# Performance work log

Measured on AMD Instinct MI355X. Metric: run time of the kernel, lower is better.

Reference implementation:

```python
import jax, jax.numpy as jnp
import numpy as np
from jax import lax

B, N, C = 16, 16384, 256          # batch, points, seed feature dim
P, NS = 256, 16                   # num_proposal, ball-query nsample
RADIUS = 0.3
NUM_CLASS, NUM_HEADING_BIN, NUM_SIZE = 18, 12, 18
OUT_FEAT = 2 + 3 + NUM_HEADING_BIN * 2 + NUM_SIZE * 4 + NUM_CLASS   # 119
PN2_NC = 128
MID_FEAT = (PN2_NC + OUT_FEAT) // 2                                 # 123
EPS = 1e-5

PARAM_NAMES = [f"mlp_{s}{i}" for i in range(3) for s in ("w", "b", "g", "be")] + [
    "c1_w", "c1_b", "bn1_g", "bn1_b", "c2_w", "c2_b", "bn2_g", "bn2_b", "c3_w", "c3_b"]


def setup_inputs():
    key = jax.random.key(0)
    ks = iter(jax.random.split(key, 32))
    def w(shape):
        return jax.random.normal(next(ks), shape, jnp.float32) / np.float32(np.sqrt(shape[0]))
    inp = {
        "pos":      jax.random.normal(next(ks), (B, N, 3), jnp.float32),
        "features": jax.random.normal(next(ks), (B, C, N), jnp.float32),
        "seed_pos": jax.random.normal(next(ks), (B, N, 3), jnp.float32),
    }
    dims = [3 + C, PN2_NC, PN2_NC, PN2_NC]
    for i in range(3):
        inp[f"mlp_w{i}"]  = w((dims[i], dims[i + 1]))
        inp[f"mlp_b{i}"]  = jnp.zeros((dims[i + 1],), jnp.float32)
        inp[f"mlp_g{i}"]  = jnp.ones((dims[i + 1],), jnp.float32)
        inp[f"mlp_be{i}"] = jnp.zeros((dims[i + 1],), jnp.float32)
    inp["c1_w"], inp["c1_b"] = w((PN2_NC, PN2_NC)), jnp.zeros((PN2_NC,), jnp.float32)
    inp["bn1_g"], inp["bn1_b"] = jnp.ones((PN2_NC,), jnp.float32), jnp.zeros((PN2_NC,), jnp.float32)
    inp["c2_w"], inp["c2_b"] = w((PN2_NC, MID_FEAT)), jnp.zeros((MID_FEAT,), jnp.float32)
    inp["bn2_g"], inp["bn2_b"] = jnp.ones((MID_FEAT,), jnp.float32), jnp.zeros((MID_FEAT,), jnp.float32)
    inp["c3_w"], inp["c3_b"] = w((MID_FEAT, OUT_FEAT)), jnp.zeros((OUT_FEAT,), jnp.float32)
    return inp


def _fps(p):
    # iterative furthest point sampling on one cloud p:[N,3] -> [P] int32 (starts at index 0)
    def step(carry, _):
        dists, far = carry
        d = jnp.sum((p - p[far]) ** 2, axis=-1)
        dists = jnp.minimum(dists, d)
        return (dists, jnp.argmax(dists).astype(jnp.int32)), far
    init = (jnp.full((p.shape[0],), 1e10, p.dtype), jnp.array(0, jnp.int32))
    _, idx = lax.scan(step, init, None, length=P)
    return idx


def _ball_query(new_pos, pos):
    # first NS points of pos within RADIUS of each center (CUDA ball_query semantics)
    d2 = jnp.sum((new_pos[:, :, None, :] - pos[:, None, :, :]) ** 2, -1)  # [B,P,N]
    n = pos.shape[1]
    ar = jnp.arange(n, dtype=jnp.int32)
    sortkey = jnp.where(d2 <= RADIUS ** 2, ar, ar + n)
    vals, idx = lax.top_k(-sortkey, NS)        # smallest keys = earliest in-radius indices
    valid = (-vals) < n
    return jnp.where(valid, idx, idx[..., :1])  # pad misses with first hit


def _bn(x, g, b, axes):
    m = jnp.mean(x, axes, keepdims=True)
    v = jnp.var(x, axes, keepdims=True)
    return (x - m) * lax.rsqrt(v + EPS) * g + b


def _forward(pos, features, seed_pos, params):
    idx_p = jax.vmap(_fps)(seed_pos)                              # seed_fps sampling [B,P]
    take = jax.vmap(lambda a, i: a[i])
    new_pos = take(pos, idx_p)                                    # [B,P,3]
    idx = _ball_query(new_pos, pos)                               # [B,P,NS]
    gp = take(pos, idx.reshape(B, -1)).reshape(B, P, NS, 3)
    gf = take(features.transpose(0, 2, 1), idx.reshape(B, -1)).reshape(B, P, NS, C)
    x = jnp.concatenate([gp - new_pos[:, :, None, :], gf], -1)    # [B,P,NS,3+C]
    for i in range(3):                                            # shared MLP (1x1 conv2d + BN + ReLU)
        x = jax.nn.relu(_bn(x @ params[f"mlp_w{i}"] + params[f"mlp_b{i}"],
                            params[f"mlp_g{i}"], params[f"mlp_be{i}"], (0, 1, 2)))
    x = jnp.max(x, axis=2)                                        # max over neighbors -> [B,P,128]
    x = jax.nn.relu(_bn(x @ params["c1_w"] + params["c1_b"], params["bn1_g"], params["bn1_b"], (0, 1)))
    x = jax.nn.relu(_bn(x @ params["c2_w"] + params["c2_b"], params["bn2_g"], params["bn2_b"], (0, 1)))
    x = x @ params["c3_w"] + params["c3_b"]                       # [B,P,OUT_FEAT]
    return x.transpose(0, 2, 1)                                   # [B,OUT_FEAT,P] like torch Conv1d


def reference(pos, features, seed_pos, mlp_w0, mlp_b0, mlp_g0, mlp_be0, mlp_w1, mlp_b1, mlp_g1, mlp_be1, mlp_w2, mlp_b2, mlp_g2, mlp_be2, c1_w, c1_b, bn1_g, bn1_b, c2_w, c2_b, bn2_g, bn2_b, c3_w, c3_b):
    ps = [mlp_w0, mlp_b0, mlp_g0, mlp_be0, mlp_w1, mlp_b1, mlp_g1, mlp_be1,
          mlp_w2, mlp_b2, mlp_g2, mlp_be2, c1_w, c1_b, bn1_g, bn1_b,
          c2_w, c2_b, bn2_g, bn2_b, c3_w, c3_b]
    params = dict(zip(PARAM_NAMES, ps))
    return _forward(pos, features, seed_pos, params)
```

## Files before the change

### kernel.cpp

```cpp
#include <hip/hip_runtime.h>

#define N_PTS 16384
#define BATCH 16
#define NPROP 256
#define NSAMP 16
#define CFEAT 256
#define KIN 259
#define KPAD 264
#define MBIG 65536
#define MSMALL 4096
#define NOUT 119
#define NBLK_BIG 512
#define NBLK_SMALL 64

#define FPS_LIST(M) M(0) M(1) M(2) M(3) M(4) M(5) M(6) M(7) \
  M(8) M(9) M(10) M(11) M(12) M(13) M(14) M(15) \
  M(16) M(17) M(18) M(19) M(20) M(21) M(22) M(23) \
  M(24) M(25) M(26) M(27) M(28) M(29) M(30) M(31)

#define FPS_PIN8(a,b,c,d,e,f,g,h) \
  asm volatile("" : "+v"(a), "+v"(b), "+v"(c), "+v"(d), \
                    "+v"(e), "+v"(f), "+v"(g), "+v"(h));

__global__ __attribute__((amdgpu_flat_work_group_size(512,512), amdgpu_waves_per_eu(2,2)))
void fps_kernel(const float* __restrict__ sp, const float* __restrict__ pos,
                int* __restrict__ idx_p, float* __restrict__ npos) {
#pragma clang fp contract(off)
  const int b = blockIdx.x;
  const int t = threadIdx.x;
  const int w = t >> 6;
  const int lane = t & 63;
  const float* base = sp + (size_t)b * N_PTS * 3;

#define FPS_DECL(J) float px##J, py##J, pz##J, dd##J;
  FPS_LIST(FPS_DECL)
#undef FPS_DECL

#define FPS_INIT(J) { const int i = t + J*512; \
    px##J = base[i*3+0]; py##J = base[i*3+1]; pz##J = base[i*3+2]; \
    dd##J = 1e10f; }
  FPS_LIST(FPS_INIT)
#undef FPS_INIT

  FPS_PIN8(px0,px1,px2,px3,px4,px5,px6,px7)
  FPS_PIN8(px8,px9,px10,px11,px12,px13,px14,px15)
  FPS_PIN8(px16,px17,px18,px19,px20,px21,px22,px23)
  FPS_PIN8(px24,px25,px26,px27,px28,px29,px30,px31)
  FPS_PIN8(py0,py1,py2,py3,py4,py5,py6,py7)
  FPS_PIN8(py8,py9,py10,py11,py12,py13,py14,py15)
  FPS_PIN8(py16,py17,py18,py19,py20,py21,py22,py23)
  FPS_PIN8(py24,py25,py26,py27,py28,py29,py30,py31)
  FPS_PIN8(pz0,pz1,pz2,pz3,pz4,pz5,pz6,pz7)
  FPS_PIN8(pz8,pz9,pz10,pz11,pz12,pz13,pz14,pz15)
  FPS_PIN8(pz16,pz17,pz18,pz19,pz20,pz21,pz22,pz23)
  FPS_PIN8(pz24,pz25,pz26,pz27,pz28,pz29,pz30,pz31)

  __shared__ unsigned long long part[2][8];
  __shared__ int sidx[NPROP];
  if (t == 0) { idx_p[b*NPROP] = 0; sidx[0] = 0; }
  float fx = base[0], fy = base[1], fz = base[2];
  for (int it = 1; it < NPROP; ++it) {
    float mv = -1.0f; int mi = 0;
#define FPS_STEP(J) { \
    float dx = px##J - fx, dy = py##J - fy, dz = pz##J - fz; \
    float d = (dx*dx + dy*dy) + dz*dz; \
    float nd = fminf(dd##J, d); \
    dd##J = nd; \
    if (nd > mv) { mv = nd; mi = t + J*512; } }
    FPS_LIST(FPS_STEP)
#undef FPS_STEP
    unsigned long long key =
      ((unsigned long long)__float_as_uint(mv) << 32) |
      (unsigned long long)(unsigned)(0x7FFFFFFF - mi);
#pragma unroll
    for (int o = 32; o > 0; o >>= 1) {
      unsigned long long ok = __shfl_xor(key, o, 64);
      if (ok > key) key = ok;
    }
    const int buf = it & 1;
    if (lane == 0) part[buf][w] = key;
    __syncthreads();
    unsigned long long k2 = part[buf][0];
#pragma unroll
    for (int q = 1; q < 8; ++q) {
      unsigned long long ok = part[buf][q];
      if (ok > k2) k2 = ok;
    }
    const int far = 0x7FFFFFFF - (int)(unsigned)(k2 & 0xFFFFFFFFull);
    if (t == 0) { idx_p[b*NPROP + it] = far; sidx[it] = far; }
    const float* fp = base + (size_t)far*3;
    fx = fp[0]; fy = fp[1]; fz = fp[2];
  }
  __syncthreads();
  if (t < NPROP) {
    const int ii = sidx[t];
    const float* pp = pos + ((size_t)b*N_PTS + ii)*3;
    float* np = npos + (size_t)(b*NPROP + t)*3;
    np[0] = pp[0]; np[1] = pp[1]; np[2] = pp[2];
  }
}

__global__ __launch_bounds__(256)
void ballq_kernel(const float* __restrict__ pos, const float* __restrict__ npos,
                  int* __restrict__ idxg) {
#pragma clang fp contract(off)
  __shared__ int res[4][NSAMP];
  const int tid = threadIdx.x;
  const int w = tid >> 6, lane = tid & 63;
  const int cid = blockIdx.x*4 + w;
  const int b = cid >> 8;
  const float R2 = (float)(0.3*0.3);
  if (lane == 0) res[w][0] = 0;
  const float cx = npos[cid*3+0], cy = npos[cid*3+1], cz = npos[cid*3+2];
  const float* pb = pos + (size_t)b*N_PTS*3;
  int cnt = 0;
  const unsigned long long lmask = (1ull << lane) - 1ull;
#pragma unroll 4
  for (int ch = 0; ch < N_PTS/64; ++ch) {
    int i = ch*64 + lane;
    float dx = pb[i*3+0]-cx, dy = pb[i*3+1]-cy, dz = pb[i*3+2]-cz;
    float d2 = (dx*dx + dy*dy) + dz*dz;
    bool pred = d2 <= R2;
    unsigned long long bal = __ballot(pred);
    if (pred) {
      int slot = cnt + (int)__popcll(bal & lmask);
      if (slot < NSAMP) res[w][slot] = i;
    }
    cnt += (int)__popcll(bal);
  }
  __syncthreads();
  if (lane < NSAMP) {
    int v = res[w][lane];
    if (lane >= cnt) v = res[w][0];
    idxg[cid*NSAMP + lane] = v;
  }
}

__global__ __launch_bounds__(256)
void prep_w(const float* __restrict__ w0, const float* __restrict__ c2w,
            const float* __restrict__ c2b, const float* __restrict__ c3w,
            const float* __restrict__ c3b,
            float* __restrict__ Wp0, float* __restrict__ Wp2, float* __restrict__ B2p,
            float* __restrict__ Wp3, float* __restrict__ B3p) {
  int g = blockIdx.x*256 + threadIdx.x;
  const int S0 = KPAD*128, S1 = S0 + 16384, S2 = S1 + 128, S3 = S2 + 16384, S4 = S3 + 128;
  if (g < S0) {
    int k = g >> 7, n = g & 127;
    Wp0[g] = (k < KIN) ? w0[k*128 + n] : 0.f;
  } else if (g < S1) {
    int g2 = g - S0; int k = g2 >> 7, n = g2 & 127;
    Wp2[g2] = (n < 123) ? c2w[k*123 + n] : 0.f;
  } else if (g < S2) {
    int n = g - S1;
    B2p[n] = (n < 123) ? c2b[n] : 0.f;
  } else if (g < S3) {
    int g2 = g - S2; int k = g2 >> 7, n = g2 & 127;
    Wp3[g2] = (k < 123 && n < NOUT) ? c3w[k*NOUT + n] : 0.f;
  } else if (g < S4) {
    int n = g - S3;
    B3p[n] = (n < NOUT) ? c3b[n] : 0.f;
  }
}

__global__ __launch_bounds__(256)
void gemm_l0(const float* __restrict__ pos, const float* __restrict__ npos,
             const float* __restrict__ feat, const int* __restrict__ idxg,
             const float* __restrict__ Wp, const float* __restrict__ bias,
             float* __restrict__ H, float* __restrict__ Sp, float* __restrict__ Qp) {
  __shared__ float As[8][128];
  __shared__ float Ws[8][128];
  __shared__ float pd[3][128];
  __shared__ int ids[128];
  const int tid = threadIdx.x;
  const int m0 = blockIdx.x * 128;
  const int b = m0 >> 12;
  const float* fb = feat + (size_t)b * CFEAT * N_PTS;
  if (tid < 128) {
    int m = m0 + tid;
    int ii = idxg[m];
    ids[tid] = ii;
    int q = m >> 4;
    const float* pp = pos + ((size_t)b*N_PTS + ii)*3;
    const float* cc = npos + (size_t)q*3;
    pd[0][tid] = pp[0] - cc[0];
    pd[1][tid] = pp[1] - cc[1];
    pd[2][tid] = pp[2] - cc[2];
  }
  __syncthreads();
  const int kr = tid >> 5;
  const int cm = (tid & 31) * 4;
  int ii_r[4];
#pragma unroll
  for (int x = 0; x < 4; ++x) ii_r[x] = ids[cm+x];
  float acc[8][8];
#pragma unroll
  for (int i = 0; i < 8; ++i)
#pragma unroll
    for (int j = 0; j < 8; ++j) acc[i][j] = 0.f;
  const int tm = tid & 15, tn = tid >> 4;
  for (int k0 = 0; k0 < KPAD; k0 += 8) {
    const int k = k0 + kr;
    float4 a0;
    if (k < 3) {
      a0.x = pd[k][cm+0]; a0.y = pd[k][cm+1]; a0.z = pd[k][cm+2]; a0.w = pd[k][cm+3];
    } else if (k < KIN) {
      const float* fr = fb + (size_t)(k-3)*N_PTS;
      a0.x = fr[ii_r[0]]; a0.y = fr[ii_r[1]]; a0.z = fr[ii_r[2]]; a0.w = fr[ii_r[3]];
    } else {
      a0 = make_float4(0.f,0.f,0.f,0.f);
    }
    float4 wv = *(const float4*)(Wp + (size_t)k*128 + cm);
    __syncthreads();
    *(float4*)&As[kr][cm] = a0;
    *(float4*)&Ws[kr][cm] = wv;
    __syncthreads();
#pragma unroll
    for (int kk = 0; kk < 8; ++kk) {
      float a[8], bb[8];
      *(float4*)(a)   = *(const float4*)&As[kk][tm*4];
      *(float4*)(a+4) = *(const float4*)&As[kk][tm*4 + 64];
      *(float4*)(bb)   = *(const float4*)&Ws[kk][tn*8];
      *(float4*)(bb+4) = *(const float4*)&Ws[kk][tn*8+4];
#pragma unroll
      for (int i = 0; i < 8; ++i)
#pragma unroll
        for (int j = 0; j < 8; ++j)
          acc[i][j] = fmaf(a[i], bb[j], acc[i][j]);
    }
  }
#pragma unroll
  for (int j = 0; j < 8; ++j) {
    const int n = tn*8 + j;
    const float bv = bias[n];
    float* cr = H + (size_t)n*MBIG + m0 + tm*4;
    float4 o0, o1;
    o0.x = acc[0][j]+bv; o0.y = acc[1][j]+bv; o0.z = acc[2][j]+bv; o0.w = acc[3][j]+bv;
    o1.x = acc[4][j]+bv; o1.y = acc[5][j]+bv; o1.z = acc[6][j]+bv; o1.w = acc[7][j]+bv;
    *(float4*)(cr)      = o0;
    *(float4*)(cr + 64) = o1;
    float s = o0.x+o0.y+o0.z+o0.w + o1.x+o1.y+o1.z+o1.w;
    float q = o0.x*o0.x+o0.y*o0.y+o0.z*o0.z+o0.w*o0.w
            + o1.x*o1.x+o1.y*o1.y+o1.z*o1.z+o1.w*o1.w;
#pragma unroll
    for (int o = 1; o < 16; o <<= 1) {
      s += __shfl_xor(s, o, 64);
      q += __shfl_xor(q, o, 64);
    }
    if (tm == 0) {
      Sp[(size_t)n*NBLK_BIG + blockIdx.x] = s;
      Qp[(size_t)n*NBLK_BIG + blockIdx.x] = q;
    }
  }
}

template<int TM, int MODE, int DOPART>
__global__ __launch_bounds__(256)
void gemm_k(const float* __restrict__ A, const float* __restrict__ W,
            const float* __restrict__ bias, const float* __restrict__ sc,
            const float* __restrict__ sh, float* __restrict__ C,
            float* __restrict__ Sp, float* __restrict__ Qp,
            int M, int K, int useT) {
  __shared__ float As[8][TM];
  __shared__ float Ws[8][128];
  const int tid = threadIdx.x;
  const int m0 = blockIdx.x * TM;
  const int kr = tid >> 5;
  const int cw = (tid & 31) * 4;
  const int tm = tid & 15, tn = tid >> 4;
  constexpr int MR = TM / 16;
  constexpr int NBLK = (TM == 128) ? NBLK_BIG : NBLK_SMALL;
  float acc[MR][8];
#pragma unroll
  for (int i = 0; i < MR; ++i)
#pragma unroll
    for (int j = 0; j < 8; ++j) acc[i][j] = 0.f;
  for (int k0 = 0; k0 < K; k0 += 8) {
    const float* ar = A + (size_t)(k0+kr)*M + m0;
    float4 wv = *(const float4*)(W + (size_t)(k0+kr)*128 + cw);
    const float s_ = useT ? sc[k0+kr] : 1.f;
    const float h_ = useT ? sh[k0+kr] : 0.f;
    if constexpr (TM == 128) {
      float4 a0 = *(const float4*)(ar + cw);
      if (useT) {
        a0.x = fmaxf(fmaf(a0.x, s_, h_), 0.f);
        a0.y = fmaxf(fmaf(a0.y, s_, h_), 0.f);
        a0.z = fmaxf(fmaf(a0.z, s_, h_), 0.f);
        a0.w = fmaxf(fmaf(a0.w, s_, h_), 0.f);
      }
      __syncthreads();
      *(float4*)&As[kr][cw] = a0;
      *(float4*)&Ws[kr][cw] = wv;
      __syncthreads();
    } else {
      const int c2 = (tid & 31) * 2;
      float2 a0 = *(const float2*)(ar + c2);
      if (useT) {
        a0.x = fmaxf(fmaf(a0.x, s_, h_), 0.f);
        a0.y = fmaxf(fmaf(a0.y, s_, h_), 0.f);
      }
      __syncthreads();
      *(float2*)&As[kr][c2] = a0;
      *(float4*)&Ws[kr][cw] = wv;
      __syncthreads();
    }
#pragma unroll
    for (int kk = 0; kk < 8; ++kk) {
      float a[MR], bb[8];
      *(float4*)(a) = *(const float4*)&As[kk][tm*4];
      if constexpr (MR == 8)
        *(float4*)(a+4) = *(const float4*)&As[kk][tm*4 + 64];
      *(float4*)(bb)   = *(const float4*)&Ws[kk][tn*8];
      *(float4*)(bb+4) = *(const float4*)&Ws[kk][tn*8+4];
#pragma unroll
      for (int i = 0; i < MR; ++i)
#pragma unroll
        for (int j = 0; j < 8; ++j)
          acc[i][j] = fmaf(a[i], bb[j], acc[i][j]);
    }
  }
  if (MODE == 0) {
#pragma unroll
    for (int j = 0; j < 8; ++j) {
      const int n = tn*8 + j;
      const float bv = bias[n];
      float* cr = C + (size_t)n*M + m0 + tm*4;
      float4 o0, o1;
      o0.x = acc[0][j]+bv; o0.y = acc[1][j]+bv; o0.z = acc[2][j]+bv; o0.w = acc[3][j]+bv;
      *(float4*)(cr) = o0;
      if constexpr (MR == 8) {
        o1.x = acc[4][j]+bv; o1.y = acc[5][j]+bv; o1.z = acc[6][j]+bv; o1.w = acc[7][j]+bv;
        *(float4*)(cr + 64) = o1;
      }
      if constexpr (DOPART) {
        float s = o0.x+o0.y+o0.z+o0.w;
        float q = o0.x*o0.x+o0.y*o0.y+o0.z*o0.z+o0.w*o0.w;
        if constexpr (MR == 8) {
          s += o1.x+o1.y+o1.z+o1.w;
          q += o1.x*o1.x+o1.y*o1.y+o1.z*o1.z+o1.w*o1.w;
        }
#pragma unroll
        for (int o = 1; o < 16; o <<= 1) {
          s += __shfl_xor(s, o, 64);
          q += __shfl_xor(q, o, 64);
        }
        if (tm == 0) {
          Sp[(size_t)n*NBLK + blockIdx.x] = s;
          Qp[(size_t)n*NBLK + blockIdx.x] = q;
        }
      }
    }
  } else {
    const int bb_ = m0 >> 8;
    const int pcol = (m0 & 255) + tm*4;
#pragma unroll
    for (int j = 0; j < 8; ++j) {
      const int n = tn*8 + j;
      if (n < NOUT) {
        const float bv = bias[n];
        float* cr = C + ((size_t)bb_*NOUT + n)*256 + pcol;
        float4 o0;
        o0.x = acc[0][j]+bv; o0.y = acc[1][j]+bv; o0.z = acc[2][j]+bv; o0.w = acc[3][j]+bv;
        *(float4*)(cr) = o0;
      }
    }
  }
}

__global__ __launch_bounds__(256)
void stats_finish(const float* __restrict__ Sp, const float* __restrict__ Qp,
                  int nblk, int M, int nc,
                  const float* __restrict__ g, const float* __restrict__ be,
                  float* __restrict__ sc, float* __restrict__ sh) {
  const int c = blockIdx.x;
  const int tid = threadIdx.x;
  if (c >= nc) { if (tid == 0) { sc[c] = 0.f; sh[c] = 0.f; } return; }
  float s = 0.f, q = 0.f;
  for (int i = tid; i < nblk; i += 256) {
    s += Sp[(size_t)c*nblk + i];
    q += Qp[(size_t)c*nblk + i];
  }
#pragma unroll
  for (int o = 32; o > 0; o >>= 1) {
    s += __shfl_xor(s, o, 64);
    q += __shfl_xor(q, o, 64);
  }
  __shared__ float ws_[4], wq_[4];
  const int w = tid >> 6, lane = tid & 63;
  if (lane == 0) { ws_[w] = s; wq_[w] = q; }
  __syncthreads();
  if (tid == 0) {
    float S = ws_[0]+ws_[1]+ws_[2]+ws_[3];
    float Q = wq_[0]+wq_[1]+wq_[2]+wq_[3];
    float mean = S / (float)M;
    float var  = Q / (float)M - mean*mean;
    float inv  = rsqrtf(var + 1e-5f);
    float gg = g[c];
    sc[c] = inv * gg;
    sh[c] = be[c] - mean * inv * gg;
  }
}

__global__ __launch_bounds__(256)
void pool_kernel(const float* __restrict__ H2, const float* __restrict__ sc,
                 const float* __restrict__ sh, float* __restrict__ X3) {
  int gidx = blockIdx.x*256 + threadIdx.x;
  int c = gidx >> 12;
  int q = gidx & 4095;
  const float* src = H2 + (size_t)c*MBIG + (size_t)q*NSAMP;
  float s_ = sc[c], h_ = sh[c];
  float m = 0.f;
#pragma unroll
  for (int k = 0; k < NSAMP; k += 4) {
    float4 v = *(const float4*)(src + k);
    m = fmaxf(m, fmaf(v.x, s_, h_));
    m = fmaxf(m, fmaf(v.y, s_, h_));
    m = fmaxf(m, fmaf(v.z, s_, h_));
    m = fmaxf(m, fmaf(v.w, s_, h_));
  }
  X3[(size_t)c*MSMALL + q] = m;
}

extern "C" void kernel_launch(void* const* d_in, const int* in_sizes, int n_in,
                              void* d_out, int out_size, void* d_ws, size_t ws_size,
                              hipStream_t stream) {
  const float* pos  = (const float*)d_in[0];
  const float* feat = (const float*)d_in[1];
  const float* spos = (const float*)d_in[2];
  const float* w0  = (const float*)d_in[3];
  const float* b0  = (const float*)d_in[4];
  const float* g0  = (const float*)d_in[5];
  const float* be0 = (const float*)d_in[6];
  const float* w1  = (const float*)d_in[7];
  const float* b1  = (const float*)d_in[8];
  const float* g1  = (const float*)d_in[9];
  const float* be1 = (const float*)d_in[10];
  const float* w2  = (const float*)d_in[11];
  const float* b2  = (const float*)d_in[12];
  const float* g2  = (const float*)d_in[13];
  const float* be2 = (const float*)d_in[14];
  const float* c1w = (const float*)d_in[15];
  const float* c1b = (const float*)d_in[16];
  const float* bg1 = (const float*)d_in[17];
  const float* bb1 = (const float*)d_in[18];
  const float* c2w = (const float*)d_in[19];
  const float* c2b = (const float*)d_in[20];
  const float* bg2 = (const float*)d_in[21];
  const float* bb2 = (const float*)d_in[22];
  const float* c3w = (const float*)d_in[23];
  const float* c3b = (const float*)d_in[24];
  float* out = (float*)d_out;

  float* fws = (float*)d_ws;
  size_t off = 0;
  auto alloc = [&](size_t n) { float* p = fws + off; off += n; return p; };
  float* H0  = alloc((size_t)128*MBIG);
  float* H1  = alloc((size_t)128*MBIG);
  float* X3  = alloc((size_t)128*MSMALL);
  float* H3  = alloc((size_t)128*MSMALL);
  float* H4  = alloc((size_t)128*MSMALL);
  float* Wp0 = alloc(KPAD*128);
  float* Wp2 = alloc(16384);
  float* B2p = alloc(128);
  float* Wp3 = alloc(16384);
  float* B3p = alloc(128);
  float* sc0 = alloc(128); float* sh0 = alloc(128);
  float* sc1 = alloc(128); float* sh1 = alloc(128);
  float* sc2 = alloc(128); float* sh2 = alloc(128);
  float* sc3 = alloc(128); float* sh3 = alloc(128);
  float* sc4 = alloc(128); float* sh4 = alloc(128);
  float* Sp  = alloc((size_t)128*NBLK_BIG);
  float* Qp  = alloc((size_t)128*NBLK_BIG);
  float* npos = alloc((size_t)BATCH*NPROP*3);
  int* idx_p = (int*)alloc(BATCH*NPROP);
  int* idxg  = (int*)alloc(MBIG);
  float* H2 = H0;

  fps_kernel<<<BATCH, 512, 0, stream>>>(spos, pos, idx_p, npos);
  ballq_kernel<<<BATCH*NPROP/4, 256, 0, stream>>>(pos, npos, idxg);
  prep_w<<<261, 256, 0, stream>>>(w0, c2w, c2b, c3w, c3b, Wp0, Wp2, B2p, Wp3, B3p);

  gemm_l0<<<MBIG/128, 256, 0, stream>>>(pos, npos, feat, idxg, Wp0, b0, H0, Sp, Qp);
  stats_finish<<<128, 256, 0, stream>>>(Sp, Qp, NBLK_BIG, MBIG, 128, g0, be0, sc0, sh0);
  gemm_k<128,0,1><<<MBIG/128, 256, 0, stream>>>(H0, w1, b1, sc0, sh0, H1, Sp, Qp, MBIG, 128, 1);
  stats_finish<<<128, 256, 0, stream>>>(Sp, Qp, NBLK_BIG, MBIG, 128, g1, be1, sc1, sh1);
  gemm_k<128,0,1><<<MBIG/128, 256, 0, stream>>>(H1, w2, b2, sc1, sh1, H2, Sp, Qp, MBIG, 128, 1);
  stats_finish<<<128, 256, 0, stream>>>(Sp, Qp, NBLK_BIG, MBIG, 128, g2, be2, sc2, sh2);
  pool_kernel<<<128*MSMALL/256, 256, 0, stream>>>(H2, sc2, sh2, X3);

  gemm_k<64,0,1><<<MSMALL/64, 256, 0, stream>>>(X3, c1w, c1b, nullptr, nullptr, H3, Sp, Qp, MSMALL, 128, 0);
  stats_finish<<<128, 256, 0, stream>>>(Sp, Qp, NBLK_SMALL, MSMALL, 128, bg1, bb1, sc3, sh3);
  gemm_k<64,0,1><<<MSMALL/64, 256, 0, stream>>>(H3, Wp2, B2p, sc3, sh3, H4, Sp, Qp, MSMALL, 128, 1);
  stats_finish<<<128, 256, 0, stream>>>(Sp, Qp, NBLK_SMALL, MSMALL, 123, bg2, bb2, sc4, sh4);
  gemm_k<64,1,0><<<MSMALL/64, 256, 0, stream>>>(H4, Wp3, B3p, sc4, sh4, out, nullptr, nullptr, MSMALL, 128, 1);
}
```

Measured before the change: 860.6 us.

## Add dedicated big-layer GEMM with resident weights and double-buffered A tiles

Adds a specialised gemm_big kernel for the two 65536x128x128 MLP layers. It loads the full 128x128 weight matrix into shared memory once, and double-buffers the A tile so the next slice's global load and BN/ReLU transform overlap the current FMA work, using one barrier per step instead of two. The generic gemm_k loses its TM==128 path, which simplifies it to the small-M case only. The trade-off is 72 KB of shared memory per block, which may limit occupancy.

New measurement: 855.8 us. About the same (-0.6%).

```diff
diff --git a/kernel.cpp b/kernel.cpp
--- a/kernel.cpp
+++ b/kernel.cpp
@@ -253,6 +253,91 @@
   }
 }
 
+__global__ __launch_bounds__(256)
+void gemm_big(const float* __restrict__ A, const float* __restrict__ W,
+              const float* __restrict__ bias, const float* __restrict__ sc,
+              const float* __restrict__ sh, float* __restrict__ C,
+              float* __restrict__ Sp, float* __restrict__ Qp) {
+  __shared__ float Ws[128][128];
+  __shared__ float As[2][8][128];
+  const int tid = threadIdx.x;
+  const int m0 = blockIdx.x * 128;
+  const int kr = tid >> 5;
+  const int cw = (tid & 31) * 4;
+  const int tm = tid & 15, tn = tid >> 4;
+#pragma unroll
+  for (int rr = 0; rr < 16; ++rr) {
+    const int k = rr*8 + kr;
+    *(float4*)&Ws[k][cw] = *(const float4*)(W + (size_t)k*128 + cw);
+  }
+  {
+    float4 a0 = *(const float4*)(A + (size_t)kr*MBIG + m0 + cw);
+    const float s_ = sc[kr], h_ = sh[kr];
+    a0.x = fmaxf(fmaf(a0.x, s_, h_), 0.f);
+    a0.y = fmaxf(fmaf(a0.y, s_, h_), 0.f);
+    a0.z = fmaxf(fmaf(a0.z, s_, h_), 0.f);
+    a0.w = fmaxf(fmaf(a0.w, s_, h_), 0.f);
+    *(float4*)&As[0][kr][cw] = a0;
+  }
+  __syncthreads();
+  float acc[8][8];
+#pragma unroll
+  for (int i = 0; i < 8; ++i)
+#pragma unroll
+    for (int j = 0; j < 8; ++j) acc[i][j] = 0.f;
+  for (int step = 0; step < 16; ++step) {
+    const int cur = step & 1;
+    float4 a1;
+    if (step < 15) {
+      const int k = (step+1)*8 + kr;
+      a1 = *(const float4*)(A + (size_t)k*MBIG + m0 + cw);
+      const float s_ = sc[k], h_ = sh[k];
+      a1.x = fmaxf(fmaf(a1.x, s_, h_), 0.f);
+      a1.y = fmaxf(fmaf(a1.y, s_, h_), 0.f);
+      a1.z = fmaxf(fmaf(a1.z, s_, h_), 0.f);
+      a1.w = fmaxf(fmaf(a1.w, s_, h_), 0.f);
+    }
+#pragma unroll
+    for (int kk = 0; kk < 8; ++kk) {
+      float a[8], bb[8];
+      *(float4*)(a)   = *(const float4*)&As[cur][kk][tm*4];
+      *(float4*)(a+4) = *(const float4*)&As[cur][kk][tm*4 + 64];
+      *(float4*)(bb)   = *(const float4*)&Ws[step*8+kk][tn*8];
+      *(float4*)(bb+4) = *(const float4*)&Ws[step*8+kk][tn*8+4];
+#pragma unroll
+      for (int i = 0; i < 8; ++i)
+#pragma unroll
+        for (int j = 0; j < 8; ++j)
+          acc[i][j] = fmaf(a[i], bb[j], acc[i][j]);
+    }
+    if (step < 15) *(float4*)&As[cur^1][kr][cw] = a1;
+    __syncthreads();
+  }
+#pragma unroll
+  for (int j = 0; j < 8; ++j) {
+    const int n = tn*8 + j;
+    const float bv = bias[n];
+    float* cr = C + (size_t)n*MBIG + m0 + tm*4;
+    float4 o0, o1;
+    o0.x = acc[0][j]+bv; o0.y = acc[1][j]+bv; o0.z = acc[2][j]+bv; o0.w = acc[3][j]+bv;
+    o1.x = acc[4][j]+bv; o1.y = acc[5][j]+bv; o1.z = acc[6][j]+bv; o1.w = acc[7][j]+bv;
+    *(float4*)(cr)      = o0;
+    *(float4*)(cr + 64) = o1;
+    float s = o0.x+o0.y+o0.z+o0.w + o1.x+o1.y+o1.z+o1.w;
+    float q = o0.x*o0.x+o0.y*o0.y+o0.z*o0.z+o0.w*o0.w
+            + o1.x*o1.x+o1.y*o1.y+o1.z*o1.z+o1.w*o1.w;
+#pragma unroll
+    for (int o = 1; o < 16; o <<= 1) {
+      s += __shfl_xor(s, o, 64);
+      q += __shfl_xor(q, o, 64);
+    }
+    if (tm == 0) {
+      Sp[(size_t)n*NBLK_BIG + blockIdx.x] = s;
+      Qp[(size_t)n*NBLK_BIG + blockIdx.x] = q;
+    }
+  }
+}
+
 template<int TM, int MODE, int DOPART>
 __global__ __launch_bounds__(256)
 void gemm_k(const float* __restrict__ A, const float* __restrict__ W,
@@ -279,36 +364,20 @@
     float4 wv = *(const float4*)(W + (size_t)(k0+kr)*128 + cw);
     const float s_ = useT ? sc[k0+kr] : 1.f;
     const float h_ = useT ? sh[k0+kr] : 0.f;
-    if constexpr (TM == 128) {
-      float4 a0 = *(const float4*)(ar + cw);
-      if (useT) {
-        a0.x = fmaxf(fmaf(a0.x, s_, h_), 0.f);
-        a0.y = fmaxf(fmaf(a0.y, s_, h_), 0.f);
-        a0.z = fmaxf(fmaf(a0.z, s_, h_), 0.f);
-        a0.w = fmaxf(fmaf(a0.w, s_, h_), 0.f);
-      }
-      __syncthreads();
-      *(float4*)&As[kr][cw] = a0;
-      *(float4*)&Ws[kr][cw] = wv;
-      __syncthreads();
-    } else {
-      const int c2 = (tid & 31) * 2;
-      float2 a0 = *(const float2*)(ar + c2);
-      if (useT) {
-        a0.x = fmaxf(fmaf(a0.x, s_, h_), 0.f);
-        a0.y = fmaxf(fmaf(a0.y, s_, h_), 0.f);
-      }
-      __syncthreads();
-      *(float2*)&As[kr][c2] = a0;
-      *(float4*)&Ws[kr][cw] = wv;
-      __syncthreads();
-    }
+    const int c2 = (tid & 31) * 2;
+    float2 a0 = *(const float2*)(ar + c2);
+    if (useT) {
+      a0.x = fmaxf(fmaf(a0.x, s_, h_), 0.f);
+      a0.y = fmaxf(fmaf(a0.y, s_, h_), 0.f);
+    }
+    __syncthreads();
+    *(float2*)&As[kr][c2] = a0;
+    *(float4*)&Ws[kr][cw] = wv;
+    __syncthreads();
 #pragma unroll
     for (int kk = 0; kk < 8; ++kk) {
       float a[MR], bb[8];
       *(float4*)(a) = *(const float4*)&As[kk][tm*4];
-      if constexpr (MR == 8)
-        *(float4*)(a+4) = *(const float4*)&As[kk][tm*4 + 64];
       *(float4*)(bb)   = *(const float4*)&Ws[kk][tn*8];
       *(float4*)(bb+4) = *(const float4*)&Ws[kk][tn*8+4];
 #pragma unroll
@@ -324,20 +393,12 @@
       const int n = tn*8 + j;
       const float bv = bias[n];
       float* cr = C + (size_t)n*M + m0 + tm*4;
-      float4 o0, o1;
+      float4 o0;
       o0.x = acc[0][j]+bv; o0.y = acc[1][j]+bv; o0.z = acc[2][j]+bv; o0.w = acc[3][j]+bv;
       *(float4*)(cr) = o0;
-      if constexpr (MR == 8) {
-        o1.x = acc[4][j]+bv; o1.y = acc[5][j]+bv; o1.z = acc[6][j]+bv; o1.w = acc[7][j]+bv;
-        *(float4*)(cr + 64) = o1;
-      }
       if constexpr (DOPART) {
         float s = o0.x+o0.y+o0.z+o0.w;
         float q = o0.x*o0.x+o0.y*o0.y+o0.z*o0.z+o0.w*o0.w;
-        if constexpr (MR == 8) {
-          s += o1.x+o1.y+o1.z+o1.w;
-          q += o1.x*o1.x+o1.y*o1.y+o1.z*o1.z+o1.w*o1.w;
-        }
 #pragma unroll
         for (int o = 1; o < 16; o <<= 1) {
           s += __shfl_xor(s, o, 64);
@@ -481,9 +542,9 @@
 
   gemm_l0<<<MBIG/128, 256, 0, stream>>>(pos, npos, feat, idxg, Wp0, b0, H0, Sp, Qp);
   stats_finish<<<128, 256, 0, stream>>>(Sp, Qp, NBLK_BIG, MBIG, 128, g0, be0, sc0, sh0);
-  gemm_k<128,0,1><<<MBIG/128, 256, 0, stream>>>(H0, w1, b1, sc0, sh0, H1, Sp, Qp, MBIG, 128, 1);
+  gemm_big<<<MBIG/128, 256, 0, stream>>>(H0, w1, b1, sc0, sh0, H1, Sp, Qp);
   stats_finish<<<128, 256, 0, stream>>>(Sp, Qp, NBLK_BIG, MBIG, 128, g1, be1, sc1, sh1);
-  gemm_k<128,0,1><<<MBIG/128, 256, 0, stream>>>(H1, w2, b2, sc1, sh1, H2, Sp, Qp, MBIG, 128, 1);
+  gemm_big<<<MBIG/128, 256, 0, stream>>>(H1, w2, b2, sc1, sh1, H2, Sp, Qp);
   stats_finish<<<128, 256, 0, stream>>>(Sp, Qp, NBLK_BIG, MBIG, 128, g2, be2, sc2, sh2);
   pool_kernel<<<128*MSMALL/256, 256, 0, stream>>>(H2, sc2, sh2, X3);
 
```
